# Kernel optimization log

Measured on AMD Instinct MI355X. Metric: run time of the kernel, lower is better.

## Reference

```python
import jax, jax.numpy as jnp
import numpy as np

B, N, C = 4, 1024, 512
HEADS, DIM_HEAD = 8, 64
DIM_E, DIM_S, DIM_H = 64, 64, 32
INNER = HEADS * DIM_HEAD


def setup_inputs() -> dict:
    key = jax.random.key(0)
    ks = jax.random.split(key, 10)
    s = 0.02
    return {
        "x": jax.random.normal(ks[0], (B, N, C), jnp.float32),
        "w_qkv": jax.random.normal(ks[1], (3 * INNER, C), jnp.float32) * s,
        "w_proj": jax.random.normal(ks[2], (C, INNER), jnp.float32) * s,
        "b_proj": jnp.zeros((C,), jnp.float32),
        "w_e": jax.random.normal(ks[3], (DIM_E, DIM_HEAD), jnp.float32) * s,
        "b_e": jax.random.normal(ks[4], (DIM_E,), jnp.float32) * s,
        "w_s": jax.random.normal(ks[5], (DIM_S, DIM_HEAD), jnp.float32) * s,
        "b_s": jax.random.normal(ks[6], (DIM_S,), jnp.float32) * s,
        "w_h": jax.random.normal(ks[7], (DIM_H, DIM_HEAD), jnp.float32) * s,
        "b_h": jax.random.normal(ks[8], (DIM_H,), jnp.float32) * s,
        "alpha": jnp.float32(1.0),
        "beta": jnp.float32(1.0),
        "gamma": jnp.float32(1.0),
        "temperature": jnp.float32(1.0),
    }


def _sqdist(a, b):
    # |a_n - b_m|^2 via expansion; a,b: (B,H,N,d) -> (B,H,N,N)
    an = jnp.sum(a * a, -1)
    bn = jnp.sum(b * b, -1)
    return an[..., :, None] + bn[..., None, :] - 2.0 * jnp.einsum("bhnd,bhmd->bhnm", a, b)


def reference(x, w_qkv, w_proj, b_proj, w_e, b_e, w_s, b_s, w_h, b_h,
              alpha, beta, gamma, temperature):
    Bx, Nx, Cx = x.shape
    dh = w_e.shape[1]
    H = (w_qkv.shape[0] // 3) // dh

    qkv = x @ w_qkv.T                      # (B,N,3*inner)
    q, k, v = jnp.split(qkv, 3, axis=-1)
    to_heads = lambda t: t.reshape(Bx, Nx, H, dh).transpose(0, 2, 1, 3)  # (B,H,N,dh)
    q, k, v = to_heads(q), to_heads(k), to_heads(v)

    # metric embeddings
    eq, ek = q @ w_e.T + b_e, k @ w_e.T + b_e
    sq, sk = q @ w_s.T + b_s, k @ w_s.T + b_s
    sq = sq / jnp.maximum(jnp.linalg.norm(sq, axis=-1, keepdims=True), 1e-12)
    sk = sk / jnp.maximum(jnp.linalg.norm(sk, axis=-1, keepdims=True), 1e-12)
    hq, hk = jnp.tanh(q @ w_h.T + b_h), jnp.tanh(k @ w_h.T + b_h)

    # Euclidean (torch.cdist p=2)
    dE = jnp.sqrt(jnp.maximum(_sqdist(eq, ek), 1e-12))
    # spherical
    sim = jnp.einsum("bhnd,bhmd->bhnm", sq, sk)
    dS = jnp.arccos(jnp.clip(sim, -1.0 + 1e-6, 1.0 - 1e-6))
    # Poincare: diff_norm_sq expanded instead of (B,H,N,N,dim_h) broadcast tensor
    un = jnp.sum(hq * hq, -1)              # (B,H,N)
    vn = jnp.sum(hk * hk, -1)
    dns = jnp.maximum(_sqdist(hq, hk), 0.0)
    denom = (1.0 - un)[..., :, None] * (1.0 - vn)[..., None, :]
    arg = jnp.maximum(1.0 + 2.0 * dns / (denom + 1e-8), 1.0 + 1e-6)
    dH = jnp.arccosh(arg)

    sp = jax.nn.softplus
    D = sp(alpha) * dE + sp(beta) * dS + sp(gamma) * dH
    attn = jax.nn.softmax(-D / sp(temperature), axis=-1)  # (B,H,N,N)

    out = jnp.einsum("bhnm,bhmd->bhnd", attn, v)
    out = out.transpose(0, 2, 1, 3).reshape(Bx, Nx, H * dh)
    return out @ w_proj.T + b_proj
```

## Files before the change

kernel.cpp:

```cpp
#include <hip/hip_runtime.h>
#include <math.h>

typedef unsigned short u16;
typedef __attribute__((ext_vector_type(8))) short short8;
typedef __attribute__((ext_vector_type(4))) short short4v;
typedef __attribute__((ext_vector_type(4))) float floatx4;

#define BB 4
#define NN 1024
#define CC 512
#define HH 8
#define INNERD 512
#define BHCNT 32
#define MTOK 4096
#define NSPLIT 2

constexpr size_t OFF_XB  = 0;
constexpr size_t OFF_WQB = 4194304;
constexpr size_t OFF_WPB = 5767168;
constexpr size_t OFF_WEB = 6291456;
constexpr size_t OFF_WSB = 6299648;
constexpr size_t OFF_WHB = 6307840;
constexpr size_t OFF_QKV = 6311936;
constexpr size_t OFF_EQ  = 18894848;
constexpr size_t OFF_EK  = 23089152;
constexpr size_t OFF_SQ  = 27283456;
constexpr size_t OFF_SK  = 31477760;
constexpr size_t OFF_HQ  = 35672064;
constexpr size_t OFF_HK  = 37769216;
constexpr size_t OFF_VT  = 39866368;
constexpr size_t OFF_EQN = 44060672;
constexpr size_t OFF_EKN = 44191744;
constexpr size_t OFF_HQN = 44322816;
constexpr size_t OFF_HKN = 44453888;
constexpr size_t OFF_AO  = 44584960;
constexpr size_t OFF_OP  = 48779264;
constexpr size_t OFF_LP  = 65556480;

#if __has_builtin(__builtin_amdgcn_exp2f)
#define FEXP2(x) __builtin_amdgcn_exp2f(x)
#else
#define FEXP2(x) exp2f(x)
#endif
#if __has_builtin(__builtin_amdgcn_logf)
#define FLOG2(x) __builtin_amdgcn_logf(x)
#else
#define FLOG2(x) log2f(x)
#endif
#if __has_builtin(__builtin_amdgcn_sqrtf)
#define FSQRT(x) __builtin_amdgcn_sqrtf(x)
#else
#define FSQRT(x) sqrtf(x)
#endif
#if __has_builtin(__builtin_amdgcn_rcpf)
#define FRCP(x) __builtin_amdgcn_rcpf(x)
#else
#define FRCP(x) (1.0f / (x))
#endif

__device__ __forceinline__ short f2bf(float f) {
    unsigned u = __float_as_uint(f);
    unsigned r = u + 0x7fffu + ((u >> 16) & 1u);
    return (short)(r >> 16);
}
__device__ __forceinline__ floatx4 mfma16(short8 a, short8 b, floatx4 c) {
    return __builtin_amdgcn_mfma_f32_16x16x32_bf16(a, b, c, 0, 0, 0);
}
__device__ __forceinline__ float softplusf(float x) { return log1pf(expf(x)); }
__device__ __forceinline__ float qsum16(float v) {
    v += __shfl_xor(v, 1); v += __shfl_xor(v, 2);
    v += __shfl_xor(v, 4); v += __shfl_xor(v, 8);
    return v;
}
__device__ __forceinline__ float ftanh(float x) {
    const float t = FEXP2(x * 2.8853900817779268f);
    return (t - 1.0f) * FRCP(t + 1.0f);
}

__global__ __launch_bounds__(256) void k0_cvt(
    const float* __restrict__ x, const float* __restrict__ wq,
    const float* __restrict__ wp, const float* __restrict__ we,
    const float* __restrict__ wsp, const float* __restrict__ whp,
    u16* __restrict__ xb, u16* __restrict__ wqb, u16* __restrict__ wpb,
    u16* __restrict__ web, u16* __restrict__ wsb, u16* __restrict__ whb) {
    const size_t i = ((size_t)blockIdx.x * 256 + threadIdx.x) * 4;
    const float* s; u16* d; size_t off;
    if (i < 2097152)      { s = x;   d = xb;  off = i; }
    else if (i < 2883584) { s = wq;  d = wqb; off = i - 2097152; }
    else if (i < 3145728) { s = wp;  d = wpb; off = i - 2883584; }
    else if (i < 3149824) { s = we;  d = web; off = i - 3145728; }
    else if (i < 3153920) { s = wsp; d = wsb; off = i - 3149824; }
    else                  { s = whp; d = whb; off = i - 3153920; }
    const float4 v = *(const float4*)(s + off);
    short4v o;
    o[0] = f2bf(v.x); o[1] = f2bf(v.y); o[2] = f2bf(v.z); o[3] = f2bf(v.w);
    *(short4v*)(d + off) = o;
}

__global__ __launch_bounds__(256) void k1_qkv(const u16* __restrict__ x,
                                              const u16* __restrict__ wqkv,
                                              u16* __restrict__ qkv) {
    __shared__ u16 sB[2][64 * 40];
    const int tm = blockIdx.x * 128;
    const int o0 = blockIdx.y * 64;
    const int tid = threadIdx.x, lane = tid & 63, w = tid >> 6;
    const int l15 = lane & 15, quad = lane >> 4;
    const int arow = tm + w * 16 + l15;
    const int brow = tid >> 2, bj = (tid & 3) * 8;
    const int bOff = brow * 40 + bj;
    const u16* bsrc = wqkv + (size_t)(o0 + brow) * CC + bj;

    floatx4 acc[2][4];
    #pragma unroll
    for (int qt = 0; qt < 2; ++qt)
        #pragma unroll
        for (int s = 0; s < 4; ++s) acc[qt][s] = (floatx4){0.f, 0.f, 0.f, 0.f};

    *(short8*)&sB[0][bOff] = *(const short8*)bsrc;
    __syncthreads();

    #pragma unroll 1
    for (int kc = 0; kc < CC / 32; ++kc) {
        const int cur = kc & 1, nxt = cur ^ 1;
        short8 pB;
        if (kc + 1 < CC / 32) pB = *(const short8*)(bsrc + (kc + 1) * 32);

        short8 a0 = *(const short8*)(x + (size_t)arow * CC + kc * 32 + quad * 8);
        short8 a1 = *(const short8*)(x + (size_t)(arow + 64) * CC + kc * 32 + quad * 8);
        #pragma unroll
        for (int s = 0; s < 4; ++s) {
            short8 b = *(const short8*)&sB[cur][(s * 16 + l15) * 40 + quad * 8];
            acc[0][s] = mfma16(a0, b, acc[0][s]);
            acc[1][s] = mfma16(a1, b, acc[1][s]);
        }
        if (kc + 1 < CC / 32) *(short8*)&sB[nxt][bOff] = pB;
        __syncthreads();
    }
    #pragma unroll
    for (int qt = 0; qt < 2; ++qt) {
        #pragma unroll
        for (int s = 0; s < 4; ++s) {
            const int o = o0 + s * 16 + l15;
            const int sq_i = o >> 9, rem = o & 511;
            const int h = rem >> 6, d = rem & 63;
            #pragma unroll
            for (int r = 0; r < 4; ++r) {
                const int tok = tm + qt * 64 + w * 16 + quad * 4 + r;
                const int bb = tok >> 10, n = tok & (NN - 1);
                qkv[((((size_t)sq_i * BB + bb) * HH + h) * NN + n) * 64 + d] =
                    (u16)f2bf(acc[qt][s][r]);
            }
        }
    }
}

__global__ __launch_bounds__(256) void k2_embed(
    const u16* __restrict__ qkv,
    const u16* __restrict__ we, const float* __restrict__ be,
    const u16* __restrict__ wsp, const float* __restrict__ bsp,
    const u16* __restrict__ whp, const float* __restrict__ bhp,
    u16* __restrict__ eq, u16* __restrict__ ek,
    u16* __restrict__ sq, u16* __restrict__ sk,
    u16* __restrict__ hq, u16* __restrict__ hk,
    float* __restrict__ eqn, float* __restrict__ ekn,
    float* __restrict__ hqn, float* __restrict__ hkn,
    u16* __restrict__ vt) {
    const int bh = blockIdx.x, n0 = blockIdx.y * 64;
    const int b = bh >> 3, h = bh & 7;
    const int tid = threadIdx.x, lane = tid & 63, w = tid >> 6;
    const int l15 = lane & 15, quad = lane >> 4;

    __shared__ u16 stgE[64][72];
    __shared__ u16 stgS[64][72];
    __shared__ u16 stgH[64][40];
    const int srow = tid >> 2;
    const int scol = (tid & 3) * 16;
    const int hcol = (tid & 3) * 8;

    for (int src = 0; src < 2; ++src) {
        const u16* qbase = qkv + (((size_t)src * BB + b) * HH + h) * NN * 64;
        const int tokA = n0 + w * 16 + l15;
        short8 afr[2];
        #pragma unroll
        for (int c = 0; c < 2; ++c)
            afr[c] = *(const short8*)(qbase + (size_t)tokA * 64 + c * 32 + quad * 8);

        floatx4 ce[4], cs[4], ch[2];
        #pragma unroll
        for (int i = 0; i < 4; ++i) { ce[i] = (floatx4){0.f,0.f,0.f,0.f}; cs[i] = (floatx4){0.f,0.f,0.f,0.f}; }
        #pragma unroll
        for (int i = 0; i < 2; ++i) ch[i] = (floatx4){0.f,0.f,0.f,0.f};

        #pragma unroll
        for (int c = 0; c < 2; ++c) {
            const int k0 = c * 32 + quad * 8;
            #pragma unroll
            for (int i = 0; i < 4; ++i) {
                short8 bf = *(const short8*)(we + (size_t)(i * 16 + l15) * 64 + k0);
                ce[i] = mfma16(afr[c], bf, ce[i]);
            }
            #pragma unroll
            for (int i = 0; i < 4; ++i) {
                short8 bf = *(const short8*)(wsp + (size_t)(i * 16 + l15) * 64 + k0);
                cs[i] = mfma16(afr[c], bf, cs[i]);
            }
            #pragma unroll
            for (int i = 0; i < 2; ++i) {
                short8 bf = *(const short8*)(whp + (size_t)(i * 16 + l15) * 64 + k0);
                ch[i] = mfma16(afr[c], bf, ch[i]);
            }
        }
        u16* edst = src ? ek : eq;
        u16* sdst = src ? sk : sq;
        u16* hdst = src ? hk : hq;
        float* endst = src ? ekn : eqn;
        float* hndst = src ? hkn : hqn;
        const int myrow = w * 16 + quad * 4;

        float epart[4] = {0.f, 0.f, 0.f, 0.f};
        #pragma unroll
        for (int i = 0; i < 4; ++i) {
            const float bias = be[i * 16 + l15];
            #pragma unroll
            for (int r = 0; r < 4; ++r) {
                const float v = ce[i][r] + bias;
                const short vb = f2bf(v);
                const float vr = __uint_as_float(((unsigned)(u16)vb) << 16);
                epart[r] += vr * vr;
                stgE[myrow + r][i * 16 + l15] = (u16)vb;
            }
        }
        #pragma unroll
        for (int r = 0; r < 4; ++r) {
            const float s = qsum16(epart[r]);
            if (l15 == 0) endst[(size_t)bh * NN + n0 + myrow + r] = s;
        }
        float sv[4][4], sn2[4] = {0.f, 0.f, 0.f, 0.f};
        #pragma unroll
        for (int i = 0; i < 4; ++i) {
            const float bias = bsp[i * 16 + l15];
            #pragma unroll
            for (int r = 0; r < 4; ++r) {
                const float v = cs[i][r] + bias;
                sv[i][r] = v;
                sn2[r] += v * v;
            }
        }
        float inv[4];
        #pragma unroll
        for (int r = 0; r < 4; ++r) {
            const float t = qsum16(sn2[r]);
            inv[r] = FRCP(fmaxf(FSQRT(t), 1e-12f));
        }
        #pragma unroll
        for (int i = 0; i < 4; ++i) {
            #pragma unroll
            for (int r = 0; r < 4; ++r)
                stgS[myrow + r][i * 16 + l15] = (u16)f2bf(sv[i][r] * inv[r]);
        }
        float hpart[4] = {0.f, 0.f, 0.f, 0.f};
        #pragma unroll
        for (int i = 0; i < 2; ++i) {
            const float bias = bhp[i * 16 + l15];
            #pragma unroll
            for (int r = 0; r < 4; ++r) {
                const float v = ftanh(ch[i][r] + bias);
                const short vb = f2bf(v);
                const float vr = __uint_as_float(((unsigned)(u16)vb) << 16);
                hpart[r] += vr * vr;
                stgH[myrow + r][i * 16 + l15] = (u16)vb;
            }
        }
        #pragma unroll
        for (int r = 0; r < 4; ++r) {
            const float s = qsum16(hpart[r]);
            if (l15 == 0) hndst[(size_t)bh * NN + n0 + myrow + r] = s;
        }
        __syncthreads();
        {
            u16* dpE = edst + ((size_t)bh * NN + n0 + srow) * 64 + scol;
            *(short8*)dpE = *(const short8*)&stgE[srow][scol];
            *(short8*)(dpE + 8) = *(const short8*)&stgE[srow][scol + 8];
            u16* dpS = sdst + ((size_t)bh * NN + n0 + srow) * 64 + scol;
            *(short8*)dpS = *(const short8*)&stgS[srow][scol];
            *(short8*)(dpS + 8) = *(const short8*)&stgS[srow][scol + 8];
            u16* dpH = hdst + ((size_t)bh * NN + n0 + srow) * 32 + hcol;
            *(short8*)dpH = *(const short8*)&stgH[srow][hcol];
        }
        __syncthreads();
    }

    {
        const u16* vbase = qkv + (((size_t)2 * BB + b) * HH + h) * NN * 64;
        const u16* p = vbase + (size_t)(n0 + srow) * 64 + scol;
        *(short8*)(&stgE[srow][scol]) = *(const short8*)p;
        *(short8*)(&stgE[srow][scol + 8]) = *(const short8*)(p + 8);
    }
    __syncthreads();
    {
        const int d = tid >> 2, nn0 = (tid & 3) * 16;
        short8 o1, o2;
        #pragma unroll
        for (int j = 0; j < 8; ++j) o1[j] = (short)stgE[nn0 + j][d];
        #pragma unroll
        for (int j = 0; j < 8; ++j) o2[j] = (short)stgE[nn0 + 8 + j][d];
        u16* dst = vt + ((size_t)bh * 64 + d) * NN + n0 + nn0;
        *(short8*)dst = o1;
        *(short8*)(dst + 8) = o2;
    }
}

__global__ __launch_bounds__(256, 2) void k3_attn(
    const u16* __restrict__ eq, const u16* __restrict__ ek,
    const u16* __restrict__ sq, const u16* __restrict__ sk,
    const u16* __restrict__ hq, const u16* __restrict__ hk,
    const float* __restrict__ eqn, const float* __restrict__ ekn,
    const float* __restrict__ hqn, const float* __restrict__ hkn,
    const u16* __restrict__ vt,
    float* __restrict__ opart, float* __restrict__ lpart,
    const float* __restrict__ pA, const float* __restrict__ pB,
    const float* __restrict__ pG, const float* __restrict__ pT) {
    __shared__ u16 sE[2][32 * 72];
    __shared__ u16 sS[2][32 * 72];
    __shared__ u16 sH[2][32 * 40];
    __shared__ u16 sV[2][64 * 40];
    __shared__ float sEN[2][32];
    __shared__ float sHN[2][32];
    __shared__ u16 plds[4][2][16][36];

    const int bh = blockIdx.x, q0b = blockIdx.y * 128, split = blockIdx.z;
    const int tid = threadIdx.x, lane = tid & 63, w = tid >> 6;
    const int l15 = lane & 15, quad = lane >> 4;
    const int q0 = q0b + w * 16;

    const float invT = 1.0f / softplusf(pT[0]);
    const float L2E = 1.4426950408889634f;
    const float kE = -softplusf(pA[0]) * invT * L2E;
    const float kS = -softplusf(pB[0]) * invT * L2E;
    const float kH2 = -softplusf(pG[0]) * invT;

    const u16* ekb = ek + (size_t)bh * NN * 64;
    const u16* skb = sk + (size_t)bh * NN * 64;
    const u16* hkb = hk + (size_t)bh * NN * 32;
    const u16* vtb = vt + (size_t)bh * 64 * NN;
    const float* eknb = ekn + (size_t)bh * NN;
    const float* hknb = hkn + (size_t)bh * NN;

    const int kt0 = split * (NN / 32 / NSPLIT);
    const int ktend = kt0 + NN / 32 / NSPLIT;
    const int mbase = kt0 * 32;

    const int eKey = tid >> 3, eJ = (tid & 7) * 8;
    const int hKey = tid >> 2, hJ = (tid & 3) * 8;
    const int vD   = tid >> 2, vJ = (tid & 3) * 8;
    const int eOff = eKey * 72 + eJ;
    const int hOff = hKey * 40 + hJ;
    const int vOff = vD * 40 + vJ;

    short8 Ea[2][2], Sa[2][2], Ha[2];
    #pragma unroll
    for (int qt = 0; qt < 2; ++qt) {
        const size_t qrow = (size_t)bh * NN + q0 + qt * 64 + l15;
        #pragma unroll
        for (int c = 0; c < 2; ++c) {
            Ea[qt][c] = *(const short8*)(eq + qrow * 64 + c * 32 + quad * 8);
            Sa[qt][c] = *(const short8*)(sq + qrow * 64 + c * 32 + quad * 8);
        }
        Ha[qt] = *(const short8*)(hq + qrow * 32 + quad * 8);
    }

    float eqn_q[2][4], hqn_q[2][4], invcq[2][4];
    #pragma unroll
    for (int qt = 0; qt < 2; ++qt) {
        #pragma unroll
        for (int r = 0; r < 4; ++r) {
            const int t = q0 + qt * 64 + quad * 4 + r;
            eqn_q[qt][r] = eqn[(size_t)bh * NN + t];
            hqn_q[qt][r] = hqn[(size_t)bh * NN + t];
            invcq[qt][r] = FRCP(1.0f - hqn_q[qt][r]);
        }
    }

    {
        short8 vE = *(const short8*)(ekb + (size_t)(mbase + eKey) * 64 + eJ);
        short8 vS = *(const short8*)(skb + (size_t)(mbase + eKey) * 64 + eJ);
        short8 vV = *(const short8*)(vtb + (size_t)vD * NN + mbase + vJ);
        *(short8*)&sE[0][eOff] = vE;
        *(short8*)&sS[0][eOff] = vS;
        *(short8*)&sV[0][vOff] = vV;
        if (tid < 128) {
            short8 vH = *(const short8*)(hkb + (size_t)(mbase + hKey) * 32 + hJ);
            *(short8*)&sH[0][hOff] = vH;
        } else if (tid < 136) {
            float4 vN = *(const float4*)(eknb + mbase + (tid - 128) * 4);
            *(float4*)&sEN[0][(tid - 128) * 4] = vN;
        } else if (tid < 144) {
            float4 vN = *(const float4*)(hknb + mbase + (tid - 136) * 4);
            *(float4*)&sHN[0][(tid - 136) * 4] = vN;
        }
        __syncthreads();
    }

    floatx4 oacc[2][4];
    #pragma unroll
    for (int qt = 0; qt < 2; ++qt)
        #pragma unroll
        for (int db = 0; db < 4; ++db) oacc[qt][db] = (floatx4){0.f, 0.f, 0.f, 0.f};
    float lsum[2][4] = {{0.f, 0.f, 0.f, 0.f}, {0.f, 0.f, 0.f, 0.f}};

    const float PI_F = 3.14159265358979f;

    #pragma unroll 1
    for (int kt = kt0; kt < ktend; ++kt) {
        const int cur = (kt - kt0) & 1, nxt = cur ^ 1;
        const bool more = (kt + 1 < ktend);

        short8 pE, pS, pV, pH;
        float4 pEN, pHN;
        if (more) {
            const int m0 = (kt + 1) * 32;
            pE = *(const short8*)(ekb + (size_t)(m0 + eKey) * 64 + eJ);
            pS = *(const short8*)(skb + (size_t)(m0 + eKey) * 64 + eJ);
            pV = *(const short8*)(vtb + (size_t)vD * NN + m0 + vJ);
            if (tid < 128) {
                pH = *(const short8*)(hkb + (size_t)(m0 + hKey) * 32 + hJ);
            } else if (tid < 136) {
                pEN = *(const float4*)(eknb + m0 + (tid - 128) * 4);
            } else if (tid < 144) {
                pHN = *(const float4*)(hknb + m0 + (tid - 136) * 4);
            }
        }

        #pragma unroll
        for (int sub = 0; sub < 2; ++sub) {
            const int row = sub * 16 + l15;
            short8 Eb0 = *(const short8*)&sE[cur][row * 72 + quad * 8];
            short8 Eb1 = *(const short8*)&sE[cur][row * 72 + 32 + quad * 8];
            short8 Sb0 = *(const short8*)&sS[cur][row * 72 + quad * 8];
            short8 Sb1 = *(const short8*)&sS[cur][row * 72 + 32 + quad * 8];
            short8 Hb  = *(const short8*)&sH[cur][row * 40 + quad * 8];

            const float ekn_m = sEN[cur][row];
            const float hkn_m = sHN[cur][row];
            const float rck = FRCP(1.0f - hkn_m);
            const float rck2 = rck + rck;

            #pragma unroll
            for (int qt = 0; qt < 2; ++qt) {
                floatx4 z = (floatx4){0.f, 0.f, 0.f, 0.f};
                floatx4 se = mfma16(Ea[qt][1], Eb1, mfma16(Ea[qt][0], Eb0, z));
                floatx4 ss = mfma16(Sa[qt][1], Sb1, mfma16(Sa[qt][0], Sb0, z));
                floatx4 sh = mfma16(Ha[qt], Hb, z);

                #pragma unroll
                for (int r = 0; r < 4; ++r) {
                    const float dE = FSQRT(fmaxf(fmaf(se[r], -2.0f, eqn_q[qt][r] + ekn_m), 1e-12f));
                    const float t = fminf(fabsf(ss[r]), 0.999999f);
                    const float pol = fmaf(fmaf(fmaf(-0.0187293f, t, 0.0742610f), t,
                                                -0.2121144f), t, 1.5707288f);
                    const float rr = FSQRT(1.0f - t) * pol;
                    const float dS = (ss[r] >= 0.0f) ? rr : (PI_F - rr);
                    const float dns = fmaxf(fmaf(sh[r], -2.0f, hqn_q[qt][r] + hkn_m), 0.0f);
                    const float arg = fmaxf(fmaf(dns * invcq[qt][r], rck2, 1.0f), 1.0f + 1e-6f);
                    const float xs = arg + FSQRT(fmaf(arg, arg, -1.0f));
                    const float lgH = FLOG2(xs);
                    const float lg2 = fmaf(dE, kE, fmaf(dS, kS, lgH * kH2));
                    const float p = FEXP2(lg2);
                    const unsigned u = __float_as_uint(p);
                    lsum[qt][r] += __uint_as_float(u & 0xffff0000u);
                    plds[w][qt][quad * 4 + r][sub * 16 + l15] = (u16)(u >> 16);
                }
            }
        }
        short8 Vb[4];
        #pragma unroll
        for (int db = 0; db < 4; ++db)
            Vb[db] = *(const short8*)&sV[cur][(db * 16 + l15) * 40 + quad * 8];
        #pragma unroll
        for (int qt = 0; qt < 2; ++qt) {
            short8 Pa = *(const short8*)(&plds[w][qt][l15][quad * 8]);
            #pragma unroll
            for (int db = 0; db < 4; ++db)
                oacc[qt][db] = mfma16(Pa, Vb[db], oacc[qt][db]);
        }

        if (more) {
            *(short8*)&sE[nxt][eOff] = pE;
            *(short8*)&sS[nxt][eOff] = pS;
            *(short8*)&sV[nxt][vOff] = pV;
            if (tid < 128) {
                *(short8*)&sH[nxt][hOff] = pH;
            } else if (tid < 136) {
                *(float4*)&sEN[nxt][(tid - 128) * 4] = pEN;
            } else if (tid < 144) {
                *(float4*)&sHN[nxt][(tid - 136) * 4] = pHN;
            }
        }
        __syncthreads();
    }

    float* obase = opart + ((size_t)split * BHCNT + bh) * NN * 64;
    #pragma unroll
    for (int qt = 0; qt < 2; ++qt) {
        #pragma unroll
        for (int db = 0; db < 4; ++db) {
            #pragma unroll
            for (int r = 0; r < 4; ++r) {
                const int t = q0 + qt * 64 + quad * 4 + r;
                obase[(size_t)t * 64 + db * 16 + l15] = oacc[qt][db][r];
            }
        }
        #pragma unroll
        for (int r = 0; r < 4; ++r) {
            const float s = qsum16(lsum[qt][r]);
            if (l15 == 0)
                lpart[((size_t)split * BHCNT + bh) * NN + q0 + qt * 64 + quad * 4 + r] = s;
        }
    }
}

__global__ __launch_bounds__(256) void k3r_reduce(
    const float* __restrict__ opart, const float* __restrict__ lpart,
    u16* __restrict__ ao) {
    const size_t gid = (size_t)blockIdx.x * 256 + threadIdx.x;
    const size_t base = gid * 4;
    const int token = (int)(base >> 6);
    const int d0 = (int)(base & 63);
    float4 acc = {0.f, 0.f, 0.f, 0.f};
    float ls = 0.f;
    #pragma unroll
    for (int s = 0; s < NSPLIT; ++s) {
        const float4 v = *(const float4*)(opart + ((size_t)s * BHCNT * NN + token) * 64 + d0);
        acc.x += v.x; acc.y += v.y; acc.z += v.z; acc.w += v.w;
        ls += lpart[(size_t)s * BHCNT * NN + token];
    }
    const float inv = FRCP(ls);
    const int bh = token >> 10, n = token & (NN - 1);
    const int b = bh >> 3, h = bh & 7;
    short4v o;
    o[0] = f2bf(acc.x * inv); o[1] = f2bf(acc.y * inv);
    o[2] = f2bf(acc.z * inv); o[3] = f2bf(acc.w * inv);
    *(short4v*)(ao + ((size_t)b * NN + n) * INNERD + h * 64 + d0) = o;
}

__global__ __launch_bounds__(256) void k4_proj(const u16* __restrict__ ao,
                                               const u16* __restrict__ wp,
                                               const float* __restrict__ bp,
                                               float* __restrict__ out) {
    __shared__ u16 sB[2][64 * 40];
    const int tm = blockIdx.x * 128;
    const int o0 = blockIdx.y * 64;
    const int tid = threadIdx.x, lane = tid & 63, w = tid >> 6;
    const int l15 = lane & 15, quad = lane >> 4;
    const int arow = tm + w * 16 + l15;
    const int brow = tid >> 2, bj = (tid & 3) * 8;
    const int bOff = brow * 40 + bj;
    const u16* bsrc = wp + (size_t)(o0 + brow) * INNERD + bj;

    floatx4 acc[2][4];
    #pragma unroll
    for (int qt = 0; qt < 2; ++qt)
        #pragma unroll
        for (int s = 0; s < 4; ++s) acc[qt][s] = (floatx4){0.f, 0.f, 0.f, 0.f};

    *(short8*)&sB[0][bOff] = *(const short8*)bsrc;
    __syncthreads();

    #pragma unroll 1
    for (int kc = 0; kc < INNERD / 32; ++kc) {
        const int cur = kc & 1, nxt = cur ^ 1;
        short8 pB;
        if (kc + 1 < INNERD / 32) pB = *(const short8*)(bsrc + (kc + 1) * 32);

        short8 a0 = *(const short8*)(ao + (size_t)arow * INNERD + kc * 32 + quad * 8);
        short8 a1 = *(const short8*)(ao + (size_t)(arow + 64) * INNERD + kc * 32 + quad * 8);
        #pragma unroll
        for (int s = 0; s < 4; ++s) {
            short8 b = *(const short8*)&sB[cur][(s * 16 + l15) * 40 + quad * 8];
            acc[0][s] = mfma16(a0, b, acc[0][s]);
            acc[1][s] = mfma16(a1, b, acc[1][s]);
        }
        if (kc + 1 < INNERD / 32) *(short8*)&sB[nxt][bOff] = pB;
        __syncthreads();
    }
    #pragma unroll
    for (int qt = 0; qt < 2; ++qt) {
        #pragma unroll
        for (int s = 0; s < 4; ++s) {
            const int o = o0 + s * 16 + l15;
            const float bias = bp[o];
            #pragma unroll
            for (int r = 0; r < 4; ++r) {
                const int tok = tm + qt * 64 + w * 16 + quad * 4 + r;
                out[(size_t)tok * CC + o] = acc[qt][s][r] + bias;
            }
        }
    }
}

extern "C" void kernel_launch(void* const* d_in, const int* in_sizes, int n_in,
                              void* d_out, int out_size, void* d_ws, size_t ws_size,
                              hipStream_t stream) {
    const float* x     = (const float*)d_in[0];
    const float* wqkv  = (const float*)d_in[1];
    const float* wproj = (const float*)d_in[2];
    const float* bproj = (const float*)d_in[3];
    const float* we    = (const float*)d_in[4];
    const float* be    = (const float*)d_in[5];
    const float* wsp   = (const float*)d_in[6];
    const float* bsp   = (const float*)d_in[7];
    const float* whp   = (const float*)d_in[8];
    const float* bhp   = (const float*)d_in[9];
    const float* pA    = (const float*)d_in[10];
    const float* pB    = (const float*)d_in[11];
    const float* pG    = (const float*)d_in[12];
    const float* pT    = (const float*)d_in[13];

    char* ws = (char*)d_ws;
    u16* xb  = (u16*)(ws + OFF_XB);
    u16* wqb = (u16*)(ws + OFF_WQB);
    u16* wpb = (u16*)(ws + OFF_WPB);
    u16* web = (u16*)(ws + OFF_WEB);
    u16* wsb = (u16*)(ws + OFF_WSB);
    u16* whb = (u16*)(ws + OFF_WHB);
    u16* qkv = (u16*)(ws + OFF_QKV);
    u16* eq = (u16*)(ws + OFF_EQ);
    u16* ek = (u16*)(ws + OFF_EK);
    u16* sq = (u16*)(ws + OFF_SQ);
    u16* sk = (u16*)(ws + OFF_SK);
    u16* hq = (u16*)(ws + OFF_HQ);
    u16* hk = (u16*)(ws + OFF_HK);
    u16* vt = (u16*)(ws + OFF_VT);
    float* eqn = (float*)(ws + OFF_EQN);
    float* ekn = (float*)(ws + OFF_EKN);
    float* hqn = (float*)(ws + OFF_HQN);
    float* hkn = (float*)(ws + OFF_HKN);
    u16* ao = (u16*)(ws + OFF_AO);
    float* opart = (float*)(ws + OFF_OP);
    float* lpart = (float*)(ws + OFF_LP);

    k0_cvt<<<3082, 256, 0, stream>>>(x, wqkv, wproj, we, wsp, whp,
                                     xb, wqb, wpb, web, wsb, whb);
    k1_qkv<<<dim3(MTOK / 128, 1536 / 64), 256, 0, stream>>>(xb, wqb, qkv);
    k2_embed<<<dim3(BHCNT, NN / 64), 256, 0, stream>>>(
        qkv, web, be, wsb, bsp, whb, bhp,
        eq, ek, sq, sk, hq, hk, eqn, ekn, hqn, hkn, vt);
    k3_attn<<<dim3(BHCNT, NN / 128, NSPLIT), 256, 0, stream>>>(
        eq, ek, sq, sk, hq, hk, eqn, ekn, hqn, hkn, vt, opart, lpart,
        pA, pB, pG, pT);
    k3r_reduce<<<(BHCNT * NN * 64 / 4) / 256, 256, 0, stream>>>(opart, lpart, ao);
    k4_proj<<<dim3(MTOK / 128, CC / 64), 256, 0, stream>>>(ao, wpb, bproj, (float*)d_out);
}
```

Measured before the change: 196.1 us.

## Prefetch GEMM A-fragments, hoist embed loads, and pack distance math into float2

The QKV and projection GEMMs now load the A-operand fragments for the next k-chunk one iteration ahead, alongside the B prefetch, so global load latency overlaps the MFMAs. The embedding kernel issues its q/k fragment and V-band loads up front instead of inside the loop and after it. The attention kernel's per-element metric distance math is rewritten over float2 vectors with elementwise fma/max/min builtins, aiming for packed FP32 instructions. This raises register pressure in each kernel, which may lower occupancy.

Measured after the change: 190.6 us. 2.8% less time.

```diff
diff --git a/kernel.cpp b/kernel.cpp
--- a/kernel.cpp
+++ b/kernel.cpp
@@ -5,6 +5,7 @@
 typedef __attribute__((ext_vector_type(8))) short short8;
 typedef __attribute__((ext_vector_type(4))) short short4v;
 typedef __attribute__((ext_vector_type(4))) float floatx4;
+typedef __attribute__((ext_vector_type(2))) float f2;
 
 #define BB 4
 #define NN 1024
@@ -58,6 +59,11 @@
 #define FRCP(x) (1.0f / (x))
 #endif
 
+#define EFMA(a,b,c) __builtin_elementwise_fma(a,b,c)
+#define EMAX(a,b)   __builtin_elementwise_max(a,b)
+#define EMIN(a,b)   __builtin_elementwise_min(a,b)
+#define EABS(a)     __builtin_elementwise_abs(a)
+
 __device__ __forceinline__ short f2bf(float f) {
     unsigned u = __float_as_uint(f);
     unsigned r = u + 0x7fffu + ((u >> 16) & 1u);
@@ -117,23 +123,30 @@
         for (int s = 0; s < 4; ++s) acc[qt][s] = (floatx4){0.f, 0.f, 0.f, 0.f};
 
     *(short8*)&sB[0][bOff] = *(const short8*)bsrc;
+    short8 a0c = *(const short8*)(x + (size_t)arow * CC + quad * 8);
+    short8 a1c = *(const short8*)(x + (size_t)(arow + 64) * CC + quad * 8);
     __syncthreads();
 
     #pragma unroll 1
     for (int kc = 0; kc < CC / 32; ++kc) {
         const int cur = kc & 1, nxt = cur ^ 1;
-        short8 pB;
-        if (kc + 1 < CC / 32) pB = *(const short8*)(bsrc + (kc + 1) * 32);
-
-        short8 a0 = *(const short8*)(x + (size_t)arow * CC + kc * 32 + quad * 8);
-        short8 a1 = *(const short8*)(x + (size_t)(arow + 64) * CC + kc * 32 + quad * 8);
+        const bool more = (kc + 1 < CC / 32);
+        short8 pB, pa0, pa1;
+        if (more) {
+            pB  = *(const short8*)(bsrc + (kc + 1) * 32);
+            pa0 = *(const short8*)(x + (size_t)arow * CC + (kc + 1) * 32 + quad * 8);
+            pa1 = *(const short8*)(x + (size_t)(arow + 64) * CC + (kc + 1) * 32 + quad * 8);
+        }
         #pragma unroll
         for (int s = 0; s < 4; ++s) {
             short8 b = *(const short8*)&sB[cur][(s * 16 + l15) * 40 + quad * 8];
-            acc[0][s] = mfma16(a0, b, acc[0][s]);
-            acc[1][s] = mfma16(a1, b, acc[1][s]);
-        }
-        if (kc + 1 < CC / 32) *(short8*)&sB[nxt][bOff] = pB;
+            acc[0][s] = mfma16(a0c, b, acc[0][s]);
+            acc[1][s] = mfma16(a1c, b, acc[1][s]);
+        }
+        if (more) {
+            *(short8*)&sB[nxt][bOff] = pB;
+            a0c = pa0; a1c = pa1;
+        }
         __syncthreads();
     }
     #pragma unroll
@@ -177,14 +190,24 @@
     const int scol = (tid & 3) * 16;
     const int hcol = (tid & 3) * 8;
 
+    short8 afr2[2][2];
+    const int tokA = n0 + w * 16 + l15;
+    #pragma unroll
     for (int src = 0; src < 2; ++src) {
         const u16* qbase = qkv + (((size_t)src * BB + b) * HH + h) * NN * 64;
-        const int tokA = n0 + w * 16 + l15;
-        short8 afr[2];
         #pragma unroll
         for (int c = 0; c < 2; ++c)
-            afr[c] = *(const short8*)(qbase + (size_t)tokA * 64 + c * 32 + quad * 8);
-
+            afr2[src][c] = *(const short8*)(qbase + (size_t)tokA * 64 + c * 32 + quad * 8);
+    }
+    short8 vband0, vband1;
+    {
+        const u16* vbase = qkv + (((size_t)2 * BB + b) * HH + h) * NN * 64;
+        const u16* p = vbase + (size_t)(n0 + srow) * 64 + scol;
+        vband0 = *(const short8*)p;
+        vband1 = *(const short8*)(p + 8);
+    }
+
+    for (int src = 0; src < 2; ++src) {
         floatx4 ce[4], cs[4], ch[2];
         #pragma unroll
         for (int i = 0; i < 4; ++i) { ce[i] = (floatx4){0.f,0.f,0.f,0.f}; cs[i] = (floatx4){0.f,0.f,0.f,0.f}; }
@@ -197,17 +220,17 @@
             #pragma unroll
             for (int i = 0; i < 4; ++i) {
                 short8 bf = *(const short8*)(we + (size_t)(i * 16 + l15) * 64 + k0);
-                ce[i] = mfma16(afr[c], bf, ce[i]);
+                ce[i] = mfma16(afr2[src][c], bf, ce[i]);
             }
             #pragma unroll
             for (int i = 0; i < 4; ++i) {
                 short8 bf = *(const short8*)(wsp + (size_t)(i * 16 + l15) * 64 + k0);
-                cs[i] = mfma16(afr[c], bf, cs[i]);
+                cs[i] = mfma16(afr2[src][c], bf, cs[i]);
             }
             #pragma unroll
             for (int i = 0; i < 2; ++i) {
                 short8 bf = *(const short8*)(whp + (size_t)(i * 16 + l15) * 64 + k0);
-                ch[i] = mfma16(afr[c], bf, ch[i]);
+                ch[i] = mfma16(afr2[src][c], bf, ch[i]);
             }
         }
         u16* edst = src ? ek : eq;
@@ -290,12 +313,8 @@
         __syncthreads();
     }
 
-    {
-        const u16* vbase = qkv + (((size_t)2 * BB + b) * HH + h) * NN * 64;
-        const u16* p = vbase + (size_t)(n0 + srow) * 64 + scol;
-        *(short8*)(&stgE[srow][scol]) = *(const short8*)p;
-        *(short8*)(&stgE[srow][scol + 8]) = *(const short8*)(p + 8);
-    }
+    *(short8*)(&stgE[srow][scol]) = vband0;
+    *(short8*)(&stgE[srow][scol + 8]) = vband1;
     __syncthreads();
     {
         const int d = tid >> 2, nn0 = (tid & 3) * 16;
@@ -339,6 +358,15 @@
     const float kS = -softplusf(pB[0]) * invT * L2E;
     const float kH2 = -softplusf(pG[0]) * invT;
 
+    const f2 kEv = {kE, kE}, kSv = {kS, kS}, kHv = {kH2, kH2};
+    const f2 m2v = {-2.f, -2.f}, e12v = {1e-12f, 1e-12f};
+    const f2 c99v = {0.999999f, 0.999999f};
+    const f2 one2 = {1.f, 1.f}, zero2 = {0.f, 0.f};
+    const f2 oneps2 = {1.f + 1e-6f, 1.f + 1e-6f}, negone2 = {-1.f, -1.f};
+    const f2 pa3v = {-0.0187293f, -0.0187293f}, pa2v = {0.0742610f, 0.0742610f};
+    const f2 pa1v = {-0.2121144f, -0.2121144f}, pa0v = {1.5707288f, 1.5707288f};
+    const float PI_F = 3.14159265358979f;
+
     const u16* ekb = ek + (size_t)bh * NN * 64;
     const u16* skb = sk + (size_t)bh * NN * 64;
     const u16* hkb = hk + (size_t)bh * NN * 32;
@@ -369,15 +397,17 @@
         Ha[qt] = *(const short8*)(hq + qrow * 32 + quad * 8);
     }
 
-    float eqn_q[2][4], hqn_q[2][4], invcq[2][4];
+    f2 eqp[2][2], hqp[2][2], icq[2][2];
     #pragma unroll
     for (int qt = 0; qt < 2; ++qt) {
         #pragma unroll
-        for (int r = 0; r < 4; ++r) {
-            const int t = q0 + qt * 64 + quad * 4 + r;
-            eqn_q[qt][r] = eqn[(size_t)bh * NN + t];
-            hqn_q[qt][r] = hqn[(size_t)bh * NN + t];
-            invcq[qt][r] = FRCP(1.0f - hqn_q[qt][r]);
+        for (int p = 0; p < 2; ++p) {
+            const int t0 = q0 + qt * 64 + quad * 4 + 2 * p;
+            const float e0 = eqn[(size_t)bh * NN + t0], e1 = eqn[(size_t)bh * NN + t0 + 1];
+            const float h0 = hqn[(size_t)bh * NN + t0], h1 = hqn[(size_t)bh * NN + t0 + 1];
+            eqp[qt][p] = (f2){e0, e1};
+            hqp[qt][p] = (f2){h0, h1};
+            icq[qt][p] = (f2){FRCP(1.0f - h0), FRCP(1.0f - h1)};
         }
     }
 
@@ -406,9 +436,7 @@
     for (int qt = 0; qt < 2; ++qt)
         #pragma unroll
         for (int db = 0; db < 4; ++db) oacc[qt][db] = (floatx4){0.f, 0.f, 0.f, 0.f};
-    float lsum[2][4] = {{0.f, 0.f, 0.f, 0.f}, {0.f, 0.f, 0.f, 0.f}};
-
-    const float PI_F = 3.14159265358979f;
+    f2 lsum2[2][2] = {{{0.f, 0.f}, {0.f, 0.f}}, {{0.f, 0.f}, {0.f, 0.f}}};
 
     #pragma unroll 1
     for (int kt = kt0; kt < ktend; ++kt) {
@@ -443,7 +471,9 @@
             const float ekn_m = sEN[cur][row];
             const float hkn_m = sHN[cur][row];
             const float rck = FRCP(1.0f - hkn_m);
-            const float rck2 = rck + rck;
+            const f2 rckv = {rck + rck, rck + rck};
+            const f2 ekn2 = {ekn_m, ekn_m};
+            const f2 hkn2 = {hkn_m, hkn_m};
 
             #pragma unroll
             for (int qt = 0; qt < 2; ++qt) {
@@ -453,22 +483,36 @@
                 floatx4 sh = mfma16(Ha[qt], Hb, z);
 
                 #pragma unroll
-                for (int r = 0; r < 4; ++r) {
-                    const float dE = FSQRT(fmaxf(fmaf(se[r], -2.0f, eqn_q[qt][r] + ekn_m), 1e-12f));
-                    const float t = fminf(fabsf(ss[r]), 0.999999f);
-                    const float pol = fmaf(fmaf(fmaf(-0.0187293f, t, 0.0742610f), t,
-                                                -0.2121144f), t, 1.5707288f);
-                    const float rr = FSQRT(1.0f - t) * pol;
-                    const float dS = (ss[r] >= 0.0f) ? rr : (PI_F - rr);
-                    const float dns = fmaxf(fmaf(sh[r], -2.0f, hqn_q[qt][r] + hkn_m), 0.0f);
-                    const float arg = fmaxf(fmaf(dns * invcq[qt][r], rck2, 1.0f), 1.0f + 1e-6f);
-                    const float xs = arg + FSQRT(fmaf(arg, arg, -1.0f));
-                    const float lgH = FLOG2(xs);
-                    const float lg2 = fmaf(dE, kE, fmaf(dS, kS, lgH * kH2));
-                    const float p = FEXP2(lg2);
-                    const unsigned u = __float_as_uint(p);
-                    lsum[qt][r] += __uint_as_float(u & 0xffff0000u);
-                    plds[w][qt][quad * 4 + r][sub * 16 + l15] = (u16)(u >> 16);
+                for (int p = 0; p < 2; ++p) {
+                    f2 se2 = {se[2 * p], se[2 * p + 1]};
+                    f2 ss2 = {ss[2 * p], ss[2 * p + 1]};
+                    f2 sh2 = {sh[2 * p], sh[2 * p + 1]};
+                    f2 d1 = EMAX(EFMA(se2, m2v, eqp[qt][p] + ekn2), e12v);
+                    f2 dE2 = {FSQRT(d1.x), FSQRT(d1.y)};
+                    f2 t2 = EMIN(EABS(ss2), c99v);
+                    f2 pol = EFMA(EFMA(EFMA(pa3v, t2, pa2v), t2, pa1v), t2, pa0v);
+                    f2 om = one2 - t2;
+                    f2 sq2 = {FSQRT(om.x), FSQRT(om.y)};
+                    f2 rr2 = sq2 * pol;
+                    f2 dS2;
+                    dS2.x = (ss2.x >= 0.f) ? rr2.x : PI_F - rr2.x;
+                    dS2.y = (ss2.y >= 0.f) ? rr2.y : PI_F - rr2.y;
+                    f2 dns2 = EMAX(EFMA(sh2, m2v, hqp[qt][p] + hkn2), zero2);
+                    f2 arg2 = EMAX(EFMA(dns2 * icq[qt][p], rckv, one2), oneps2);
+                    f2 qa = EFMA(arg2, arg2, negone2);
+                    f2 sq3 = {FSQRT(qa.x), FSQRT(qa.y)};
+                    f2 xs2 = arg2 + sq3;
+                    f2 lgH2 = {FLOG2(xs2.x), FLOG2(xs2.y)};
+                    f2 lg2v = EFMA(dE2, kEv, EFMA(dS2, kSv, lgH2 * kHv));
+                    const float p0 = FEXP2(lg2v.x);
+                    const float p1 = FEXP2(lg2v.y);
+                    const unsigned u0 = __float_as_uint(p0);
+                    const unsigned u1 = __float_as_uint(p1);
+                    f2 tr = {__uint_as_float(u0 & 0xffff0000u),
+                             __uint_as_float(u1 & 0xffff0000u)};
+                    lsum2[qt][p] += tr;
+                    plds[w][qt][quad * 4 + 2 * p][sub * 16 + l15] = (u16)(u0 >> 16);
+                    plds[w][qt][quad * 4 + 2 * p + 1][sub * 16 + l15] = (u16)(u1 >> 16);
                 }
             }
         }
@@ -512,7 +556,8 @@
         }
         #pragma unroll
         for (int r = 0; r < 4; ++r) {
-            const float s = qsum16(lsum[qt][r]);
+            const float lv = (r & 1) ? lsum2[qt][r >> 1].y : lsum2[qt][r >> 1].x;
+            const float s = qsum16(lv);
             if (l15 == 0)
                 lpart[((size_t)split * BHCNT + bh) * NN + q0 + qt * 64 + quad * 4 + r] = s;
         }
@@ -564,23 +609,30 @@
         for (int s = 0; s < 4; ++s) acc[qt][s] = (floatx4){0.f, 0.f, 0.f, 0.f};
 
     *(short8*)&sB[0][bOff] = *(const short8*)bsrc;
+    short8 a0c = *(const short8*)(ao + (size_t)arow * INNERD + quad * 8);
+    short8 a1c = *(const short8*)(ao + (size_t)(arow + 64) * INNERD + quad * 8);
     __syncthreads();
 
     #pragma unroll 1
     for (int kc = 0; kc < INNERD / 32; ++kc) {
         const int cur = kc & 1, nxt = cur ^ 1;
-        short8 pB;
-        if (kc + 1 < INNERD / 32) pB = *(const short8*)(bsrc + (kc + 1) * 32);
-
-        short8 a0 = *(const short8*)(ao + (size_t)arow * INNERD + kc * 32 + quad * 8);
-        short8 a1 = *(const short8*)(ao + (size_t)(arow + 64) * INNERD + kc * 32 + quad * 8);
+        const bool more = (kc + 1 < INNERD / 32);
+        short8 pB, pa0, pa1;
+        if (more) {
+            pB  = *(const short8*)(bsrc + (kc + 1) * 32);
+            pa0 = *(const short8*)(ao + (size_t)arow * INNERD + (kc + 1) * 32 + quad * 8);
+            pa1 = *(const short8*)(ao + (size_t)(arow + 64) * INNERD + (kc + 1) * 32 + quad * 8);
+        }
         #pragma unroll
         for (int s = 0; s < 4; ++s) {
             short8 b = *(const short8*)&sB[cur][(s * 16 + l15) * 40 + quad * 8];
-            acc[0][s] = mfma16(a0, b, acc[0][s]);
-            acc[1][s] = mfma16(a1, b, acc[1][s]);
-        }
-        if (kc + 1 < INNERD / 32) *(short8*)&sB[nxt][bOff] = pB;
+            acc[0][s] = mfma16(a0c, b, acc[0][s]);
+            acc[1][s] = mfma16(a1c, b, acc[1][s]);
+        }
+        if (more) {
+            *(short8*)&sB[nxt][bOff] = pB;
+            a0c = pa0; a1c = pa1;
+        }
         __syncthreads();
     }
     #pragma unroll
```
